# Performance work log

Measured on AMD Instinct MI355X. Metric: run time of the kernel, lower is better.

Reference implementation:

```python
import jax, jax.numpy as jnp
import numpy as np

B, T, C = 256, 2048, 64  # batch, max_seq_len, num_classes


def setup_inputs() -> dict:
    key = jax.random.key(0)
    k1, k2, k3, k4 = jax.random.split(key, 4)
    pad_x = jax.random.normal(k1, (B, T, C), dtype=jnp.float32)
    transitions = jax.random.uniform(k2, (C, C), dtype=jnp.float32)
    origination = jax.random.uniform(k3, (C,), dtype=jnp.float32)
    batch_sizes = jnp.sort(jax.random.randint(k4, (B,), 1, T + 1))
    # the torch implementation assumes features are zero-padded past the length
    mask = jnp.arange(T)[None, :] < batch_sizes[:, None]  # (B, T)
    pad_x = pad_x * mask[:, :, None]
    return {"pad_x": pad_x, "transitions": transitions,
            "origination": origination, "batch_sizes": batch_sizes}


def reference(pad_x, transitions, origination, batch_sizes):
    # Linear-chain CRF forward algorithm (faithful to torch _forward_algo,
    # including the final sum over classes rather than logsumexp).
    x_tbc = jnp.swapaxes(pad_x, 0, 1)  # (T, B, C)
    alpha0 = x_tbc[0] + origination[None, :]  # (B, C)

    def step(alpha_prev, x_t):
        # scores[b, j, k] = alpha_prev[b, k] + transitions[j, k]
        scores = alpha_prev[:, None, :] + transitions[None, :, :]  # (B, C, C)
        alpha = x_t + jax.nn.logsumexp(scores, axis=2)  # (B, C)
        return alpha, alpha

    _, alphas_rest = jax.lax.scan(step, alpha0, x_tbc[1:])
    alphas = jnp.concatenate([alpha0[None], alphas_rest], axis=0)  # (T, B, C)
    # gather alpha at the last valid timestep of each sequence
    final = alphas[batch_sizes - 1, jnp.arange(pad_x.shape[0])]  # (B, C)
    return final.sum(axis=1)  # (B,)
```

## Files before the change

kernel.cpp:

```cpp
#include <hip/hip_runtime.h>


#define CC 64

typedef short bf16x8 __attribute__((ext_vector_type(8)));
typedef float f32x4 __attribute__((ext_vector_type(4)));

union PackAB { int w[4]; bf16x8 v; };

__device__ __forceinline__ int cvtpk(float lo, float hi) {
    int r;
    asm("v_cvt_pk_bf16_f32 %0, %1, %2" : "=v"(r) : "v"(lo), "v"(hi));
    return r;
}
__device__ __forceinline__ float bcast0(float v) {
    return __int_as_float(__builtin_amdgcn_readfirstlane(__float_as_int(v)));
}

#define LDS_FENCE() asm volatile("s_waitcnt lgkmcnt(0)" ::: "memory")

template <bool SCALE>
__device__ __forceinline__ void chain_step(const bf16x8 (&A)[4][2], PackAB (&Bf)[2][4],
                                           const f32x4* __restrict__ er4, int g,
                                           float r_, float& ns0) {
    f32x4 er[4];
    #pragma unroll
    for (int mt = 0; mt < 4; ++mt) {
        er[mt] = er4[4 * mt + g];
        if (SCALE) er[mt] *= r_;
    }

    f32x4 D[4][4];
    #pragma unroll
    for (int nt = 0; nt < 4; ++nt) {
        f32x4 Z = {0.f, 0.f, 0.f, 0.f};
        #pragma unroll
        for (int mt = 0; mt < 4; ++mt)
            D[nt][mt] = __builtin_amdgcn_mfma_f32_16x16x32_bf16(A[mt][0], Bf[0][nt].v, Z, 0, 0, 0);
    }
    #pragma unroll
    for (int nt = 0; nt < 4; ++nt)
        #pragma unroll
        for (int mt = 0; mt < 4; ++mt)
            D[nt][mt] = __builtin_amdgcn_mfma_f32_16x16x32_bf16(A[mt][1], Bf[1][nt].v, D[nt][mt], 0, 0, 0);

    ns0 = D[0][0][0];

    #pragma unroll
    for (int nt = 0; nt < 4; ++nt) {
        f32x4 d0 = D[nt][0] * er[0];
        f32x4 d1 = D[nt][1] * er[1];
        f32x4 d2 = D[nt][2] * er[2];
        f32x4 d3 = D[nt][3] * er[3];
        Bf[0][nt].w[0] = cvtpk(d0[0], d0[1]);
        Bf[0][nt].w[1] = cvtpk(d0[2], d0[3]);
        Bf[0][nt].w[2] = cvtpk(d1[0], d1[1]);
        Bf[0][nt].w[3] = cvtpk(d1[2], d1[3]);
        Bf[1][nt].w[0] = cvtpk(d2[0], d2[1]);
        Bf[1][nt].w[1] = cvtpk(d2[2], d2[3]);
        Bf[1][nt].w[2] = cvtpk(d3[0], d3[1]);
        Bf[1][nt].w[3] = cvtpk(d3[2], d3[3]);
    }
}

__launch_bounds__(64, 3)
__global__ void crf_seg_kernel(const float* __restrict__ x,
                               const float* __restrict__ trans,
                               const int*   __restrict__ lens,
                               unsigned short* __restrict__ Mws,
                               float* __restrict__ Ls,
                               int T, int Pseg, int NBshift, int SEG) {
    const int blk = blockIdx.x;
    const int b = blk >> NBshift;
    const int j = blk & ((1 << NBshift) - 1);
    const int NB = 1 << NBshift;
    const int L = lens[b];

    const int l = threadIdx.x;
    const int c = l & 15, g = l >> 4;
    const float L2E = 1.4426950408889634f;
    const float* xb = x + (size_t)b * T * CC;

    __shared__ float xl[32][CC];

    bf16x8 A[4][2];
    #pragma unroll
    for (int mt = 0; mt < 4; ++mt) {
        const float* tr = trans + (16 * mt + c) * CC;
        #pragma unroll
        for (int ch = 0; ch < 2; ++ch) {
            float4 u = *(const float4*)(tr + 32 * ch + 4 * g);
            float4 v = *(const float4*)(tr + 32 * ch + 16 + 4 * g);
            PackAB pk;
            pk.w[0] = cvtpk(__builtin_amdgcn_exp2f(u.x * L2E), __builtin_amdgcn_exp2f(u.y * L2E));
            pk.w[1] = cvtpk(__builtin_amdgcn_exp2f(u.z * L2E), __builtin_amdgcn_exp2f(u.w * L2E));
            pk.w[2] = cvtpk(__builtin_amdgcn_exp2f(v.x * L2E), __builtin_amdgcn_exp2f(v.y * L2E));
            pk.w[3] = cvtpk(__builtin_amdgcn_exp2f(v.z * L2E), __builtin_amdgcn_exp2f(v.w * L2E));
            A[mt][ch] = pk.v;
        }
    }
    PackAB Bid[2][4];
    #pragma unroll
    for (int ch = 0; ch < 2; ++ch)
        #pragma unroll
        for (int nt = 0; nt < 4; ++nt)
            #pragma unroll
            for (int qq = 0; qq < 4; ++qq) {
                int i0 = 2 * qq, i1 = 2 * qq + 1;
                int k0 = 32 * ch + 4 * g + (i0 & 3) + 16 * (i0 >> 2);
                int k1 = 32 * ch + 4 * g + (i1 & 3) + 16 * (i1 >> 2);
                Bid[ch][nt].w[qq] = cvtpk((k0 == 16 * nt + c) ? 1.f : 0.f,
                                          (k1 == 16 * nt + c) ? 1.f : 0.f);
            }

    for (int s = j; s < Pseg; s += NB) {
        const int tbeg = s * SEG;
        int segend = (s + 1) * SEG; if (segend > L - 1) segend = L - 1;
        const int nsteps = segend - tbeg;
        if (nsteps <= 0) break;

        {
            const int rl = l >> 4;
            const int cl = (l & 15) * 4;
            LDS_FENCE();
            f32x4 st[8];
            #pragma unroll
            for (int i = 0; i < 8; ++i) {
                int tr = tbeg + 1 + 4 * i + rl;
                if (tr > segend) tr = segend;
                st[i] = *(const f32x4*)(xb + (size_t)tr * CC + cl);
            }
            #pragma unroll
            for (int i = 0; i < 8; ++i) {
                f32x4 e;
                #pragma unroll
                for (int r = 0; r < 4; ++r)
                    e[r] = __builtin_amdgcn_exp2f(st[i][r] * L2E);
                *(f32x4*)&xl[4 * i + rl][cl] = e;
            }
            LDS_FENCE();
        }

        PackAB Bf[2][4];
        #pragma unroll
        for (int ch = 0; ch < 2; ++ch)
            #pragma unroll
            for (int nt = 0; nt < 4; ++nt) Bf[ch][nt] = Bid[ch][nt];

        float Lseg = 0.f, ns0 = 1.0f;
        for (int base = 0; base < nsteps; base += 4) {
            float r_ = 1.0f;
            if (base > 0) {
                float S00 = bcast0(ns0);
                r_ = __builtin_amdgcn_rcpf(S00);
                Lseg -= __builtin_amdgcn_logf(r_);
            }
            chain_step<true >(A, Bf, (const f32x4*)&xl[base][0], g, r_, ns0);
            if (base + 1 < nsteps) chain_step<false>(A, Bf, (const f32x4*)&xl[base + 1][0], g, 1.f, ns0);
            if (base + 2 < nsteps) chain_step<false>(A, Bf, (const f32x4*)&xl[base + 2][0], g, 1.f, ns0);
            if (base + 3 < nsteps) chain_step<false>(A, Bf, (const f32x4*)&xl[base + 3][0], g, 1.f, ns0);
        }

        unsigned short* Mo = Mws + ((size_t)b * Pseg + s) * 4096;
        #pragma unroll
        for (int ch = 0; ch < 2; ++ch)
            #pragma unroll
            for (int nt = 0; nt < 4; ++nt)
                #pragma unroll
                for (int e = 0; e < 8; ++e) {
                    unsigned wb = (unsigned)Bf[ch][nt].w[e >> 1];
                    unsigned short hb = (e & 1) ? (unsigned short)(wb >> 16)
                                                : (unsigned short)(wb & 0xffffu);
                    int row = 32 * ch + 4 * g + (e & 3) + 16 * (e >> 2);
                    Mo[row * 64 + 16 * nt + c] = hb;
                }
        if (l == 0) Ls[(size_t)b * Pseg + s] = Lseg;
    }
}

__launch_bounds__(64, 1)
__global__ void crf_apply_kernel(const float* __restrict__ x,
                                 const float* __restrict__ orig,
                                 const int*   __restrict__ lens,
                                 const unsigned short* __restrict__ Mws,
                                 const float* __restrict__ Ls,
                                 float* __restrict__ out,
                                 int T, int Pseg, int SEG) {
    const int b = blockIdx.x, j = threadIdx.x;
    __shared__ float qb[CC];
    const float L2E = 1.4426950408889634f, LN2 = 0.6931471805599453f;
    const int L = lens[b];
    const float* xb = x + (size_t)b * T * CC;

    float Mbar = (xb[0] + orig[0]) * L2E;
    float q = __builtin_amdgcn_exp2f((xb[j] + orig[j]) * L2E - Mbar);

    uint4 R[8];
    {
        const uint4* Ms = (const uint4*)(Mws + ((size_t)b * Pseg + 0) * 4096 + j * 64);
        #pragma unroll
        for (int i = 0; i < 8; ++i) R[i] = Ms[i];
    }

    for (int s = 0; s < Pseg; ++s) {
        int tbeg = s * SEG;
        int segend = (s + 1) * SEG; if (segend > L - 1) segend = L - 1;
        if (segend - tbeg <= 0) break;

        uint4 Rc[8];
        #pragma unroll
        for (int i = 0; i < 8; ++i) Rc[i] = R[i];
        {
            int s2 = (s + 1 < Pseg) ? s + 1 : s;
            const uint4* Ms = (const uint4*)(Mws + ((size_t)b * Pseg + s2) * 4096 + j * 64);
            #pragma unroll
            for (int i = 0; i < 8; ++i) R[i] = Ms[i];
        }

        qb[j] = q;
        LDS_FENCE();

        float acc = 0.f;
        #pragma unroll
        for (int i = 0; i < 8; ++i) {
            f32x4 qv0 = *(const f32x4*)&qb[8 * i];
            f32x4 qv1 = *(const f32x4*)&qb[8 * i + 4];
            unsigned u0 = Rc[i].x, u1 = Rc[i].y, u2 = Rc[i].z, u3 = Rc[i].w;
            acc = fmaf(__uint_as_float(u0 << 16),        qv0[0], acc);
            acc = fmaf(__uint_as_float(u0 & 0xffff0000), qv0[1], acc);
            acc = fmaf(__uint_as_float(u1 << 16),        qv0[2], acc);
            acc = fmaf(__uint_as_float(u1 & 0xffff0000), qv0[3], acc);
            acc = fmaf(__uint_as_float(u2 << 16),        qv1[0], acc);
            acc = fmaf(__uint_as_float(u2 & 0xffff0000), qv1[1], acc);
            acc = fmaf(__uint_as_float(u3 << 16),        qv1[2], acc);
            acc = fmaf(__uint_as_float(u3 & 0xffff0000), qv1[3], acc);
        }
        float S = acc;
        Mbar += Ls[(size_t)b * Pseg + s];
        float p = bcast0(S);
        float r = __builtin_amdgcn_rcpf(p);
        float lgr = __builtin_amdgcn_logf(r);
        q = S * r;
        Mbar -= lgr;
        LDS_FENCE();
    }

    float alpha = LN2 * (Mbar + __builtin_amdgcn_logf(q));
    alpha += __shfl_xor(alpha, 1, 64);
    alpha += __shfl_xor(alpha, 2, 64);
    alpha += __shfl_xor(alpha, 4, 64);
    alpha += __shfl_xor(alpha, 8, 64);
    alpha += __shfl_xor(alpha, 16, 64);
    alpha += __shfl_xor(alpha, 32, 64);
    if (j == 0) out[b] = alpha;
}

extern "C" void kernel_launch(void* const* d_in, const int* in_sizes, int n_in,
                              void* d_out, int out_size, void* d_ws, size_t ws_size,
                              hipStream_t stream) {
    const float* x     = (const float*)d_in[0];
    const float* trans = (const float*)d_in[1];
    const float* orig  = (const float*)d_in[2];
    const int*   lens  = (const int*)d_in[3];
    float* out = (float*)d_out;

    const int B = in_sizes[3];
    const int T = in_sizes[0] / (B * CC);

    int P = 64;
    while (P > 16 && ws_size < (size_t)B * P * (4096 * 2 + 4)) P >>= 1;
    const int SEG = (T + P - 1) / P;
    const int NBshift = 4;

    unsigned short* Mws = (unsigned short*)d_ws;
    float* Ls = (float*)(Mws + (size_t)B * P * 4096);

    crf_seg_kernel<<<B * 16, 64, 0, stream>>>(x, trans, lens, Mws, Ls,
                                              T, P, NBshift, SEG);
    crf_apply_kernel<<<B, 64, 0, stream>>>(x, orig, lens, Mws, Ls, out, T, P, SEG);
}
```

Measured before the change: 193.3 us.

## Replace static segment assignment with atomic work-queue dynamic scheduling

```diff
diff --git a/kernel.cpp b/kernel.cpp
--- a/kernel.cpp
+++ b/kernel.cpp
@@ -69,17 +69,11 @@
                                const int*   __restrict__ lens,
                                unsigned short* __restrict__ Mws,
                                float* __restrict__ Ls,
-                               int T, int Pseg, int NBshift, int SEG) {
-    const int blk = blockIdx.x;
-    const int b = blk >> NBshift;
-    const int j = blk & ((1 << NBshift) - 1);
-    const int NB = 1 << NBshift;
-    const int L = lens[b];
-
+                               int* __restrict__ wq,
+                               int T, int Pseg, int SEG, int ntasks) {
     const int l = threadIdx.x;
     const int c = l & 15, g = l >> 4;
     const float L2E = 1.4426950408889634f;
-    const float* xb = x + (size_t)b * T * CC;
 
     __shared__ float xl[32][CC];
 
@@ -113,11 +107,21 @@
                                           (k1 == 16 * nt + c) ? 1.f : 0.f);
             }
 
-    for (int s = j; s < Pseg; s += NB) {
+    while (true) {
+        int t;
+        if (l == 0) t = atomicAdd(wq, 1);
+        t = __shfl(t, 0, 64);
+        if (t >= ntasks) break;
+
+        const int b = t >> 6;
+        const int s = t & (Pseg - 1);
+        const int L = lens[b];
         const int tbeg = s * SEG;
         int segend = (s + 1) * SEG; if (segend > L - 1) segend = L - 1;
         const int nsteps = segend - tbeg;
-        if (nsteps <= 0) break;
+        if (nsteps <= 0) continue;
+
+        const float* xb = x + (size_t)b * T * CC;
 
         {
             const int rl = l >> 4;
@@ -161,7 +165,7 @@
             if (base + 3 < nsteps) chain_step<false>(A, Bf, (const f32x4*)&xl[base + 3][0], g, 1.f, ns0);
         }
 
-        unsigned short* Mo = Mws + ((size_t)b * Pseg + s) * 4096;
+        unsigned short* Mo = Mws + (size_t)t * 4096;
         #pragma unroll
         for (int ch = 0; ch < 2; ++ch)
             #pragma unroll
@@ -174,7 +178,7 @@
                     int row = 32 * ch + 4 * g + (e & 3) + 16 * (e >> 2);
                     Mo[row * 64 + 16 * nt + c] = hb;
                 }
-        if (l == 0) Ls[(size_t)b * Pseg + s] = Lseg;
+        if (l == 0) Ls[t] = Lseg;
     }
 }
 
@@ -267,15 +271,17 @@
     const int B = in_sizes[3];
     const int T = in_sizes[0] / (B * CC);
 
-    int P = 64;
-    while (P > 16 && ws_size < (size_t)B * P * (4096 * 2 + 4)) P >>= 1;
+    const int P = 64;
     const int SEG = (T + P - 1) / P;
-    const int NBshift = 4;
+    const int ntasks = B * P;
 
     unsigned short* Mws = (unsigned short*)d_ws;
     float* Ls = (float*)(Mws + (size_t)B * P * 4096);
-
-    crf_seg_kernel<<<B * 16, 64, 0, stream>>>(x, trans, lens, Mws, Ls,
-                                              T, P, NBshift, SEG);
+    int* wq = (int*)(Ls + ntasks);
+
+    hipMemsetAsync(wq, 0, sizeof(int), stream);
+
+    crf_seg_kernel<<<4096, 64, 0, stream>>>(x, trans, lens, Mws, Ls, wq,
+                                            T, P, SEG, ntasks);
     crf_apply_kernel<<<B, 64, 0, stream>>>(x, orig, lens, Mws, Ls, out, T, P, SEG);
 }
```

Result: slower. 289.0 us (+49.5%).
